# Performance work log

Measured on AMD Instinct MI355X. Metric: run time of the kernel, lower is better.

## Reference

```python
import jax, jax.numpy as jnp
import numpy as np

N_NODES = 50000
N_EDGES = 800000
DIM = 64
HIDDEN = 256


def setup_inputs() -> dict:
    key = jax.random.key(0)
    k_h, k_src, k_dst, k_w1, k_w2 = jax.random.split(key, 5)
    h = jax.random.normal(k_h, (N_NODES, DIM), dtype=jnp.float32)
    src = jax.random.randint(k_src, (N_EDGES,), 0, N_NODES, dtype=jnp.int64)
    dst = jax.random.randint(k_dst, (N_EDGES,), 0, N_NODES, dtype=jnp.int64)
    edge_index = jnp.stack([src, dst], axis=0)
    # Kaiming-ish init scale for the MLP weights
    W1 = jax.random.normal(k_w1, (2 * DIM, HIDDEN), dtype=jnp.float32) * (1.0 / np.sqrt(2 * DIM))
    b1 = jnp.zeros((HIDDEN,), dtype=jnp.float32)
    W2 = jax.random.normal(k_w2, (HIDDEN, DIM), dtype=jnp.float32) * (1.0 / np.sqrt(HIDDEN))
    b2 = jnp.zeros((DIM,), dtype=jnp.float32)
    return {"h": h, "edge_index": edge_index, "W1": W1, "b1": b1, "W2": W2, "b2": b2}


def reference(h, edge_index, W1, b1, W2, b2):
    n = h.shape[0]
    src, dst = edge_index[0], edge_index[1]
    # scatter-sum of neighbor features and degree counts into dst nodes
    agg = jax.ops.segment_sum(h[src], dst, num_segments=n)          # [N, D]
    deg = jax.ops.segment_sum(jnp.ones((src.shape[0],), h.dtype), dst, num_segments=n)  # [N]
    mean = agg / jnp.maximum(deg, 1.0)[:, None]
    # isolated nodes (deg == 0) keep their own features
    agg = jnp.where((deg == 0)[:, None], h, mean)
    x = jnp.concatenate([h, agg], axis=-1)                          # [N, 2D]
    # 2-layer MLP with exact (erf) GELU, matching torch nn.GELU default
    hid = jax.nn.gelu(x @ W1 + b1, approximate=False)               # [N, H]
    return hid @ W2 + b2                                            # [N, D]
```

## Files before the change

### kernel.cpp

```cpp
#include <hip/hip_runtime.h>
#include <cstdint>

#define N_NODES 50000
#define N_EDGES 800000
#define DIM 64
#define HIDDEN 256

#define NCB 196
#define EPA 2048
#define ABLKS ((N_EDGES + EPA - 1) / EPA)
#define MAXBE 5120

typedef __attribute__((ext_vector_type(8))) short bf16x8;
typedef __attribute__((ext_vector_type(4))) float f32x4;

__device__ __forceinline__ unsigned short bf16_rne(float f) {
    union { float f; uint32_t u; } cv; cv.f = f;
    uint32_t u = cv.u;
    u += 0x7FFFu + ((u >> 16) & 1u);
    return (unsigned short)(u >> 16);
}

__device__ __forceinline__ float bf2f(unsigned short us) {
    union { uint32_t u; float f; } cv; cv.u = ((uint32_t)us) << 16;
    return cv.f;
}

__device__ __forceinline__ float gelu_f(float v) {
    float u = v * (0.7978845608028654f + 0.035677408136300125f * v * v);
    float e = __expf(fmaxf(fminf(2.0f * u, 80.0f), -80.0f));
    float th = (e - 1.0f) / (e + 1.0f);
    return 0.5f * v * (1.0f + th);
}

#define PREP_TOTAL (N_NODES * DIM + 128 * 256 + 256 * 64)
__global__ __launch_bounds__(256)
void prep_kernel(const float* __restrict__ h, const float* __restrict__ W1,
                 const float* __restrict__ W2, unsigned short* __restrict__ xb,
                 unsigned short* __restrict__ w1t, unsigned short* __restrict__ w2t,
                 int* __restrict__ bcnt) {
    if (blockIdx.x == 0 && threadIdx.x < NCB) bcnt[threadIdx.x] = 0;
    int i = blockIdx.x * 256 + threadIdx.x;
    if (i < N_NODES * DIM) {
        int node = i >> 6, d = i & 63;
        xb[node * 128 + d] = bf16_rne(h[i]);
    } else if (i < N_NODES * DIM + 128 * 256) {
        int j = i - N_NODES * DIM;
        int k = j >> 8, n = j & 255;
        w1t[n * 128 + k] = bf16_rne(W1[j]);
    } else if (i < PREP_TOTAL) {
        int j = i - N_NODES * DIM - 128 * 256;
        int jr = j >> 6, d = j & 63;
        w2t[d * 256 + jr] = bf16_rne(W2[j]);
    }
}

__global__ __launch_bounds__(256)
void partA_kernel(const int* __restrict__ src, const int* __restrict__ dst,
                  int* __restrict__ bcnt, unsigned int* __restrict__ gbuf) {
    __shared__ unsigned int pairs[EPA];
    __shared__ int cnt[NCB], offs[NCB], wc[NCB], gbase[NCB];

    const int t = threadIdx.x;
    for (int i = t; i < NCB; i += 256) cnt[i] = 0;
    __syncthreads();

    const int base = blockIdx.x * EPA;
    const int ne = (N_EDGES - base < EPA) ? (N_EDGES - base) : EPA;

    #pragma unroll
    for (int i = 0; i < EPA / 256; ++i) {
        int e = t + i * 256;
        if (e < ne) atomicAdd(&cnt[((unsigned)dst[base + e]) >> 8], 1);
    }
    __syncthreads();

    if (t < 64) {
        const int b4 = t * 4;
        int c0 = (b4     < NCB) ? cnt[b4]     : 0;
        int c1 = (b4 + 1 < NCB) ? cnt[b4 + 1] : 0;
        int c2 = (b4 + 2 < NCB) ? cnt[b4 + 2] : 0;
        int c3 = (b4 + 3 < NCB) ? cnt[b4 + 3] : 0;
        const int s = c0 + c1 + c2 + c3;
        int inc = s;
        #pragma unroll
        for (int off = 1; off < 64; off <<= 1) {
            int u = __shfl_up(inc, off, 64);
            if (t >= off) inc += u;
        }
        int ex = inc - s;
        if (b4     < NCB) { offs[b4]     = ex;                wc[b4]     = ex; }
        if (b4 + 1 < NCB) { offs[b4 + 1] = ex + c0;           wc[b4 + 1] = ex + c0; }
        if (b4 + 2 < NCB) { offs[b4 + 2] = ex + c0 + c1;      wc[b4 + 2] = ex + c0 + c1; }
        if (b4 + 3 < NCB) { offs[b4 + 3] = ex + c0 + c1 + c2; wc[b4 + 3] = ex + c0 + c1 + c2; }
    }
    __syncthreads();

    #pragma unroll
    for (int i = 0; i < EPA / 256; ++i) {
        int e = t + i * 256;
        if (e < ne) {
            unsigned int d_ = (unsigned)dst[base + e];
            unsigned int p = (d_ << 16) | (unsigned)src[base + e];
            int pos = atomicAdd(&wc[d_ >> 8], 1);
            pairs[pos] = p;
        }
    }
    __syncthreads();

    if (t < NCB) {
        int c = cnt[t];
        gbase[t] = c ? (t * MAXBE + atomicAdd(&bcnt[t], c)) : 0;
    }
    __syncthreads();

    for (int p = t; p < ne; p += 256) {
        unsigned int pr = pairs[p];
        int b = (int)(pr >> 24);
        int idx = gbase[b] + (p - offs[b]);
        if (idx < (b + 1) * MAXBE) gbuf[idx] = pr;
    }
}

__global__ __launch_bounds__(1024)
void partB_kernel(const unsigned int* __restrict__ gbuf, const int* __restrict__ bcnt,
                  unsigned short* __restrict__ csr16, int2* __restrict__ rng) {
    __shared__ unsigned int ep[MAXBE];
    __shared__ unsigned int so[MAXBE];
    __shared__ int cnt[256], offs[256], wc[256];

    const int t = threadIdx.x;
    const int b = blockIdx.x;
    if (t < 256) cnt[t] = 0;
    __syncthreads();

    const int s0 = b * MAXBE;
    int ne = bcnt[b];
    if (ne > MAXBE) ne = MAXBE;

    for (int i = t; i < ne; i += 1024) {
        unsigned int p = gbuf[s0 + i];
        ep[i] = p;
        atomicAdd(&cnt[(p >> 16) & 255], 1);
    }
    __syncthreads();

    if (t < 64) {
        const int b4 = t * 4;
        int c0 = cnt[b4], c1 = cnt[b4 + 1], c2 = cnt[b4 + 2], c3 = cnt[b4 + 3];
        const int s = c0 + c1 + c2 + c3;
        int inc = s;
        #pragma unroll
        for (int off = 1; off < 64; off <<= 1) {
            int u = __shfl_up(inc, off, 64);
            if (t >= off) inc += u;
        }
        int ex = inc - s;
        offs[b4] = ex;                    wc[b4] = ex;
        offs[b4 + 1] = ex + c0;           wc[b4 + 1] = ex + c0;
        offs[b4 + 2] = ex + c0 + c1;      wc[b4 + 2] = ex + c0 + c1;
        offs[b4 + 3] = ex + c0 + c1 + c2; wc[b4 + 3] = ex + c0 + c1 + c2;
    }
    __syncthreads();

    for (int i = t; i < ne; i += 1024) {
        unsigned int p = ep[i];
        int pos = atomicAdd(&wc[(p >> 16) & 255], 1);
        so[pos] = p;
    }
    __syncthreads();

    for (int i = t; i < ne; i += 1024)
        csr16[s0 + i] = (unsigned short)(so[i] & 0xFFFFu);

    if (t < 256) {
        int node = b * 256 + t;
        if (node < N_NODES) {
            int st = s0 + offs[t];
            rng[node] = make_int2(st, st + cnt[t]);
        }
    }
}

__global__ __launch_bounds__(256)
void gather_kernel(const int2* __restrict__ rng,
                   const unsigned short* __restrict__ csr16,
                   unsigned short* __restrict__ xb) {
    int node = blockIdx.x * 4 + (threadIdx.x >> 6);
    if (node >= N_NODES) return;
    int d = threadIdx.x & 63;
    int2 rg = rng[node];
    int start = rg.x, end = rg.y;
    int degc = end - start;
    float acc = 0.0f;
    int i = start;
    for (; i + 7 < end; i += 8) {
        int s0 = csr16[i],     s1 = csr16[i + 1], s2 = csr16[i + 2], s3 = csr16[i + 3];
        int s4 = csr16[i + 4], s5 = csr16[i + 5], s6 = csr16[i + 6], s7 = csr16[i + 7];
        float v0 = bf2f(xb[(size_t)s0 * 128 + d]);
        float v1 = bf2f(xb[(size_t)s1 * 128 + d]);
        float v2 = bf2f(xb[(size_t)s2 * 128 + d]);
        float v3 = bf2f(xb[(size_t)s3 * 128 + d]);
        float v4 = bf2f(xb[(size_t)s4 * 128 + d]);
        float v5 = bf2f(xb[(size_t)s5 * 128 + d]);
        float v6 = bf2f(xb[(size_t)s6 * 128 + d]);
        float v7 = bf2f(xb[(size_t)s7 * 128 + d]);
        acc += ((v0 + v1) + (v2 + v3)) + ((v4 + v5) + (v6 + v7));
    }
    for (; i + 3 < end; i += 4) {
        int s0 = csr16[i], s1 = csr16[i + 1], s2 = csr16[i + 2], s3 = csr16[i + 3];
        float v0 = bf2f(xb[(size_t)s0 * 128 + d]);
        float v1 = bf2f(xb[(size_t)s1 * 128 + d]);
        float v2 = bf2f(xb[(size_t)s2 * 128 + d]);
        float v3 = bf2f(xb[(size_t)s3 * 128 + d]);
        acc += (v0 + v1) + (v2 + v3);
    }
    for (; i < end; ++i) acc += bf2f(xb[(size_t)csr16[i] * 128 + d]);
    unsigned short res;
    if (degc > 0) res = bf16_rne(acc / (float)degc);
    else          res = xb[(size_t)node * 128 + d];
    xb[(size_t)node * 128 + 64 + d] = res;
}

__global__ __launch_bounds__(256, 4)
void mlp_mfma_kernel(const unsigned short* __restrict__ xb,
                     const unsigned short* __restrict__ w1t,
                     const unsigned short* __restrict__ w2t,
                     const float* __restrict__ b1v,
                     const float* __restrict__ b2v,
                     float* __restrict__ out) {
    __shared__ unsigned short hid[32][264];

    const int tid = threadIdx.x;
    const int w   = tid >> 6;
    const int l   = tid & 63;
    const int l15 = l & 15;
    const int kg  = l >> 4;
    const int node0 = blockIdx.x * 32;

    int arow[2];
    #pragma unroll
    for (int nt = 0; nt < 2; ++nt) {
        int r = node0 + nt * 16 + l15;
        arow[nt] = (r < N_NODES) ? r : (N_NODES - 1);
    }

    f32x4 acc[2][4];
    #pragma unroll
    for (int a = 0; a < 2; ++a)
        #pragma unroll
        for (int b = 0; b < 4; ++b) acc[a][b] = f32x4{0.f, 0.f, 0.f, 0.f};

    #pragma unroll
    for (int s = 0; s < 4; ++s) {
        const int kofs = s * 32 + kg * 8;
        bf16x8 a[2], b[4];
        #pragma unroll
        for (int nt = 0; nt < 2; ++nt)
            a[nt] = *(const bf16x8*)(xb + (size_t)arow[nt] * 128 + kofs);
        #pragma unroll
        for (int jt = 0; jt < 4; ++jt)
            b[jt] = *(const bf16x8*)(w1t + ((w * 4 + jt) * 16 + l15) * 128 + kofs);
        #pragma unroll
        for (int nt = 0; nt < 2; ++nt)
            #pragma unroll
            for (int jt = 0; jt < 4; ++jt)
                acc[nt][jt] = __builtin_amdgcn_mfma_f32_16x16x32_bf16(
                    a[nt], b[jt], acc[nt][jt], 0, 0, 0);
    }

    #pragma unroll
    for (int jt = 0; jt < 4; ++jt) {
        const int jcol = (w * 4 + jt) * 16 + l15;
        float bias = b1v[jcol];
        #pragma unroll
        for (int nt = 0; nt < 2; ++nt) {
            #pragma unroll
            for (int r = 0; r < 4; ++r) {
                float v = acc[nt][jt][r] + bias;
                hid[nt * 16 + kg * 4 + r][jcol] = bf16_rne(gelu_f(v));
            }
        }
    }
    __syncthreads();

    f32x4 acc2[2];
    #pragma unroll
    for (int a = 0; a < 2; ++a) acc2[a] = f32x4{0.f, 0.f, 0.f, 0.f};

    #pragma unroll
    for (int s = 0; s < 8; ++s) {
        const int kofs = s * 32 + kg * 8;
        bf16x8 bb = *(const bf16x8*)(w2t + (w * 16 + l15) * 256 + kofs);
        #pragma unroll
        for (int nt = 0; nt < 2; ++nt) {
            bf16x8 aa = *(const bf16x8*)&hid[nt * 16 + l15][kofs];
            acc2[nt] = __builtin_amdgcn_mfma_f32_16x16x32_bf16(aa, bb, acc2[nt], 0, 0, 0);
        }
    }

    float bias2 = b2v[w * 16 + l15];
    #pragma unroll
    for (int nt = 0; nt < 2; ++nt) {
        #pragma unroll
        for (int r = 0; r < 4; ++r) {
            int node = node0 + nt * 16 + kg * 4 + r;
            if (node < N_NODES)
                out[(size_t)node * DIM + w * 16 + l15] = acc2[nt][r] + bias2;
        }
    }
}

extern "C" void kernel_launch(void* const* d_in, const int* in_sizes, int n_in,
                              void* d_out, int out_size, void* d_ws, size_t ws_size,
                              hipStream_t stream) {
    const float* h  = (const float*)d_in[0];
    const int* eidx = (const int*)d_in[1];
    const float* W1 = (const float*)d_in[2];
    const float* b1 = (const float*)d_in[3];
    const float* W2 = (const float*)d_in[4];
    const float* b2 = (const float*)d_in[5];
    float* out = (float*)d_out;

    const int* src = eidx;
    const int* dst = eidx + N_EDGES;

    unsigned short* xb    = (unsigned short*)d_ws;
    unsigned short* w1t   = xb + (size_t)N_NODES * 128;
    unsigned short* w2t   = w1t + 128 * 256;
    unsigned int*   gbuf  = (unsigned int*)(w2t + 256 * 64);
    unsigned short* csr16 = (unsigned short*)(gbuf + NCB * MAXBE);
    int*  bcnt = (int*)(csr16 + NCB * MAXBE);
    int2* rng  = (int2*)(bcnt + NCB + 2);

    prep_kernel<<<(PREP_TOTAL + 255) / 256, 256, 0, stream>>>(h, W1, W2, xb, w1t, w2t, bcnt);
    partA_kernel<<<ABLKS, 256, 0, stream>>>(src, dst, bcnt, gbuf);
    partB_kernel<<<NCB, 1024, 0, stream>>>(gbuf, bcnt, csr16, rng);
    {
        int grid = (N_NODES + 3) / 4;
        gather_kernel<<<grid, 256, 0, stream>>>(rng, csr16, xb);
    }
    {
        int grid = (N_NODES + 31) / 32;
        mlp_mfma_kernel<<<grid, 256, 0, stream>>>(xb, w1t, w2t, b1, b2, out);
    }
}
```

Before: 91.79 us.

## Fuse neighbor-mean gather into MLP kernel and vectorize prep conversion

Removes the standalone gather kernel. The MLP kernel now computes each node's neighbor mean itself and stages the concatenated [h, mean] rows for 32 nodes in shared memory, which feeds the MFMA A operand. The bf16 node buffer shrinks to 64 columns, so the mean no longer makes a global write-and-read round trip. The prep kernel converts four floats per thread with vector loads and stores. In exchange, the fused kernel's occupancy is limited by LDS use and launch bounds, so the latency-bound gather now runs with fewer waves, and each wave walks 8 nodes serially.

```diff
diff --git a/kernel.cpp b/kernel.cpp
--- a/kernel.cpp
+++ b/kernel.cpp
@@ -40,18 +40,29 @@
                  unsigned short* __restrict__ w1t, unsigned short* __restrict__ w2t,
                  int* __restrict__ bcnt) {
     if (blockIdx.x == 0 && threadIdx.x < NCB) bcnt[threadIdx.x] = 0;
-    int i = blockIdx.x * 256 + threadIdx.x;
-    if (i < N_NODES * DIM) {
-        int node = i >> 6, d = i & 63;
-        xb[node * 128 + d] = bf16_rne(h[i]);
-    } else if (i < N_NODES * DIM + 128 * 256) {
-        int j = i - N_NODES * DIM;
+    int i4 = (blockIdx.x * 256 + threadIdx.x) * 4;
+    if (i4 < N_NODES * DIM) {
+        float4 v = *(const float4*)&h[i4];
+        ushort4 o;
+        o.x = bf16_rne(v.x); o.y = bf16_rne(v.y);
+        o.z = bf16_rne(v.z); o.w = bf16_rne(v.w);
+        *(ushort4*)&xb[i4] = o;
+    } else if (i4 < N_NODES * DIM + 128 * 256) {
+        int j = i4 - N_NODES * DIM;
+        float4 v = *(const float4*)&W1[j];
         int k = j >> 8, n = j & 255;
-        w1t[n * 128 + k] = bf16_rne(W1[j]);
-    } else if (i < PREP_TOTAL) {
-        int j = i - N_NODES * DIM - 128 * 256;
+        w1t[(n    ) * 128 + k] = bf16_rne(v.x);
+        w1t[(n + 1) * 128 + k] = bf16_rne(v.y);
+        w1t[(n + 2) * 128 + k] = bf16_rne(v.z);
+        w1t[(n + 3) * 128 + k] = bf16_rne(v.w);
+    } else if (i4 < PREP_TOTAL) {
+        int j = i4 - N_NODES * DIM - 128 * 256;
+        float4 v = *(const float4*)&W2[j];
         int jr = j >> 6, d = j & 63;
-        w2t[d * 256 + jr] = bf16_rne(W2[j]);
+        w2t[(d    ) * 256 + jr] = bf16_rne(v.x);
+        w2t[(d + 1) * 256 + jr] = bf16_rne(v.y);
+        w2t[(d + 2) * 256 + jr] = bf16_rne(v.z);
+        w2t[(d + 3) * 256 + jr] = bf16_rne(v.w);
     }
 }
 
@@ -182,53 +193,16 @@
     }
 }
 
-__global__ __launch_bounds__(256)
-void gather_kernel(const int2* __restrict__ rng,
-                   const unsigned short* __restrict__ csr16,
-                   unsigned short* __restrict__ xb) {
-    int node = blockIdx.x * 4 + (threadIdx.x >> 6);
-    if (node >= N_NODES) return;
-    int d = threadIdx.x & 63;
-    int2 rg = rng[node];
-    int start = rg.x, end = rg.y;
-    int degc = end - start;
-    float acc = 0.0f;
-    int i = start;
-    for (; i + 7 < end; i += 8) {
-        int s0 = csr16[i],     s1 = csr16[i + 1], s2 = csr16[i + 2], s3 = csr16[i + 3];
-        int s4 = csr16[i + 4], s5 = csr16[i + 5], s6 = csr16[i + 6], s7 = csr16[i + 7];
-        float v0 = bf2f(xb[(size_t)s0 * 128 + d]);
-        float v1 = bf2f(xb[(size_t)s1 * 128 + d]);
-        float v2 = bf2f(xb[(size_t)s2 * 128 + d]);
-        float v3 = bf2f(xb[(size_t)s3 * 128 + d]);
-        float v4 = bf2f(xb[(size_t)s4 * 128 + d]);
-        float v5 = bf2f(xb[(size_t)s5 * 128 + d]);
-        float v6 = bf2f(xb[(size_t)s6 * 128 + d]);
-        float v7 = bf2f(xb[(size_t)s7 * 128 + d]);
-        acc += ((v0 + v1) + (v2 + v3)) + ((v4 + v5) + (v6 + v7));
-    }
-    for (; i + 3 < end; i += 4) {
-        int s0 = csr16[i], s1 = csr16[i + 1], s2 = csr16[i + 2], s3 = csr16[i + 3];
-        float v0 = bf2f(xb[(size_t)s0 * 128 + d]);
-        float v1 = bf2f(xb[(size_t)s1 * 128 + d]);
-        float v2 = bf2f(xb[(size_t)s2 * 128 + d]);
-        float v3 = bf2f(xb[(size_t)s3 * 128 + d]);
-        acc += (v0 + v1) + (v2 + v3);
-    }
-    for (; i < end; ++i) acc += bf2f(xb[(size_t)csr16[i] * 128 + d]);
-    unsigned short res;
-    if (degc > 0) res = bf16_rne(acc / (float)degc);
-    else          res = xb[(size_t)node * 128 + d];
-    xb[(size_t)node * 128 + 64 + d] = res;
-}
-
 __global__ __launch_bounds__(256, 4)
-void mlp_mfma_kernel(const unsigned short* __restrict__ xb,
-                     const unsigned short* __restrict__ w1t,
-                     const unsigned short* __restrict__ w2t,
-                     const float* __restrict__ b1v,
-                     const float* __restrict__ b2v,
-                     float* __restrict__ out) {
+void gmlp_kernel(const unsigned short* __restrict__ xb,
+                 const int2* __restrict__ rng,
+                 const unsigned short* __restrict__ csr16,
+                 const unsigned short* __restrict__ w1t,
+                 const unsigned short* __restrict__ w2t,
+                 const float* __restrict__ b1v,
+                 const float* __restrict__ b2v,
+                 float* __restrict__ out) {
+    __shared__ unsigned short xs[32][136];
     __shared__ unsigned short hid[32][264];
 
     const int tid = threadIdx.x;
@@ -238,12 +212,46 @@
     const int kg  = l >> 4;
     const int node0 = blockIdx.x * 32;
 
-    int arow[2];
-    #pragma unroll
-    for (int nt = 0; nt < 2; ++nt) {
-        int r = node0 + nt * 16 + l15;
-        arow[nt] = (r < N_NODES) ? r : (N_NODES - 1);
-    }
+    for (int ni = 0; ni < 8; ++ni) {
+        const int n = w * 8 + ni;
+        const int node = node0 + n;
+        float hv = 0.0f;
+        int st = 0, en = 0;
+        if (node < N_NODES) {
+            hv = bf2f(xb[(size_t)node * 64 + l]);
+            int2 rg = rng[node];
+            st = rg.x; en = rg.y;
+        }
+        float acc = 0.0f;
+        int i = st;
+        for (; i + 7 < en; i += 8) {
+            int s0 = csr16[i],     s1 = csr16[i + 1], s2 = csr16[i + 2], s3 = csr16[i + 3];
+            int s4 = csr16[i + 4], s5 = csr16[i + 5], s6 = csr16[i + 6], s7 = csr16[i + 7];
+            float v0 = bf2f(xb[(size_t)s0 * 64 + l]);
+            float v1 = bf2f(xb[(size_t)s1 * 64 + l]);
+            float v2 = bf2f(xb[(size_t)s2 * 64 + l]);
+            float v3 = bf2f(xb[(size_t)s3 * 64 + l]);
+            float v4 = bf2f(xb[(size_t)s4 * 64 + l]);
+            float v5 = bf2f(xb[(size_t)s5 * 64 + l]);
+            float v6 = bf2f(xb[(size_t)s6 * 64 + l]);
+            float v7 = bf2f(xb[(size_t)s7 * 64 + l]);
+            acc += ((v0 + v1) + (v2 + v3)) + ((v4 + v5) + (v6 + v7));
+        }
+        for (; i + 3 < en; i += 4) {
+            int s0 = csr16[i], s1 = csr16[i + 1], s2 = csr16[i + 2], s3 = csr16[i + 3];
+            float v0 = bf2f(xb[(size_t)s0 * 64 + l]);
+            float v1 = bf2f(xb[(size_t)s1 * 64 + l]);
+            float v2 = bf2f(xb[(size_t)s2 * 64 + l]);
+            float v3 = bf2f(xb[(size_t)s3 * 64 + l]);
+            acc += (v0 + v1) + (v2 + v3);
+        }
+        for (; i < en; ++i) acc += bf2f(xb[(size_t)csr16[i] * 64 + l]);
+        const int degc = en - st;
+        float mv = (degc > 0) ? (acc / (float)degc) : hv;
+        xs[n][l]      = bf16_rne(hv);
+        xs[n][64 + l] = bf16_rne(mv);
+    }
+    __syncthreads();
 
     f32x4 acc[2][4];
     #pragma unroll
@@ -257,7 +265,7 @@
         bf16x8 a[2], b[4];
         #pragma unroll
         for (int nt = 0; nt < 2; ++nt)
-            a[nt] = *(const bf16x8*)(xb + (size_t)arow[nt] * 128 + kofs);
+            a[nt] = *(const bf16x8*)&xs[nt * 16 + l15][kofs];
         #pragma unroll
         for (int jt = 0; jt < 4; ++jt)
             b[jt] = *(const bf16x8*)(w1t + ((w * 4 + jt) * 16 + l15) * 128 + kofs);
@@ -326,22 +334,18 @@
     const int* dst = eidx + N_EDGES;
 
     unsigned short* xb    = (unsigned short*)d_ws;
-    unsigned short* w1t   = xb + (size_t)N_NODES * 128;
+    unsigned short* w1t   = xb + (size_t)N_NODES * 64;
     unsigned short* w2t   = w1t + 128 * 256;
     unsigned int*   gbuf  = (unsigned int*)(w2t + 256 * 64);
     unsigned short* csr16 = (unsigned short*)(gbuf + NCB * MAXBE);
     int*  bcnt = (int*)(csr16 + NCB * MAXBE);
-    int2* rng  = (int2*)(bcnt + NCB + 2);
-
-    prep_kernel<<<(PREP_TOTAL + 255) / 256, 256, 0, stream>>>(h, W1, W2, xb, w1t, w2t, bcnt);
+    int2* rng  = (int2*)(bcnt + NCB);
+
+    prep_kernel<<<(PREP_TOTAL / 4 + 255) / 256, 256, 0, stream>>>(h, W1, W2, xb, w1t, w2t, bcnt);
     partA_kernel<<<ABLKS, 256, 0, stream>>>(src, dst, bcnt, gbuf);
     partB_kernel<<<NCB, 1024, 0, stream>>>(gbuf, bcnt, csr16, rng);
     {
-        int grid = (N_NODES + 3) / 4;
-        gather_kernel<<<grid, 256, 0, stream>>>(rng, csr16, xb);
-    }
-    {
         int grid = (N_NODES + 31) / 32;
-        mlp_mfma_kernel<<<grid, 256, 0, stream>>>(xb, w1t, w2t, b1, b2, out);
-    }
-}
+        gmlp_kernel<<<grid, 256, 0, stream>>>(xb, rng, csr16, w1t, w2t, b1, b2, out);
+    }
+}
```

Result: slower. 103.3 us (+12.6%).
